# Optimization experiments

Measured on AMD Instinct MI355X. Metric: run time of the kernel, lower is better.

Reference implementation:

```python
import jax, jax.numpy as jnp
import numpy as np

B, N, P2, D, L, K = 256, 256, 64, 128, 2, 9  # batch, nodes, patch^2, embed_dim, vig blocks, knn edges
FFN = 4 * D


def _ln(x, g, b, eps=1e-5):
    m = jnp.mean(x, -1, keepdims=True)
    v = jnp.mean((x - m) ** 2, -1, keepdims=True)
    return (x - m) / jnp.sqrt(v + eps) * g + b


def _lrelu(x):
    return jnp.where(x >= 0, x, 0.01 * x)


def _vig_block(x, mask, mf, fc1_w, fc1_b, conv_w, conv_b, fc2_w, fc2_b, f1_w, f1_b, f2_w, f2_b):
    # Grapher: fc1 -> dynamic kNN -> max-relative graph conv -> fc2, residual
    sc = x
    h = x @ fc1_w + fc1_b  # [B,N,D]
    # pairwise squared distances in feature space; masked nodes excluded as neighbors
    x2 = jnp.sum(h * h, -1)
    d2 = x2[:, :, None] + x2[:, None, :] - 2.0 * jnp.einsum('bnd,bmd->bnm', h, h)
    d2 = jnp.where(mask[:, None, :], d2, 1e10)
    _, idx = jax.lax.top_k(-d2, K)  # [B,N,K] nearest-neighbor indices (non-diff)
    Bq, Nq, Dq = h.shape
    hj = jnp.take_along_axis(h, idx.reshape(Bq, Nq * K, 1), axis=1).reshape(Bq, Nq, K, Dq)
    vj = jnp.take_along_axis(mask, idx.reshape(Bq, Nq * K), axis=1).reshape(Bq, Nq, K)
    rel = jnp.where(vj[..., None], hj - h[:, :, None, :], -1e9)
    mrel = jnp.where(vj.any(2)[..., None], rel.max(2), 0.0)  # max-relative aggregation
    h = _lrelu(jnp.concatenate([h, mrel], -1) @ conv_w + conv_b)
    x = (h @ fc2_w + fc2_b) + sc
    # FFN, residual (drop_path = identity at eval)
    sc = x
    x = _lrelu(x @ f1_w + f1_b) @ f2_w + f2_b + sc
    return x * mf


def setup_inputs() -> dict:
    key = jax.random.key(0)
    ks = jax.random.split(key, 32)
    s = 0.02
    d = {
        'nodes_batch': jax.random.normal(ks[0], (B, N, P2), jnp.float32),
        'node_mask': jax.random.randint(ks[1], (B, N), 0, 2) > 0,
        'emb_w1': jax.random.normal(ks[2], (P2, 2 * D), jnp.float32) * s,
        'emb_b1': jnp.zeros((2 * D,), jnp.float32),
        'emb_ln1_g': jnp.ones((2 * D,), jnp.float32),
        'emb_ln1_b': jnp.zeros((2 * D,), jnp.float32),
        'emb_w2': jax.random.normal(ks[3], (2 * D, D), jnp.float32) * s,
        'emb_b2': jnp.zeros((D,), jnp.float32),
        'emb_ln2_g': jnp.ones((D,), jnp.float32),
        'emb_ln2_b': jnp.zeros((D,), jnp.float32),
        'vig_fc1_w': jax.random.normal(ks[4], (L, D, D), jnp.float32) * s,
        'vig_fc1_b': jnp.zeros((L, D), jnp.float32),
        'vig_conv_w': jax.random.normal(ks[5], (L, 2 * D, D), jnp.float32) * s,
        'vig_conv_b': jnp.zeros((L, D), jnp.float32),
        'vig_fc2_w': jax.random.normal(ks[6], (L, D, D), jnp.float32) * s,
        'vig_fc2_b': jnp.zeros((L, D), jnp.float32),
        'vig_ffn1_w': jax.random.normal(ks[7], (L, D, FFN), jnp.float32) * s,
        'vig_ffn1_b': jnp.zeros((L, FFN), jnp.float32),
        'vig_ffn2_w': jax.random.normal(ks[8], (L, FFN, D), jnp.float32) * s,
        'vig_ffn2_b': jnp.zeros((L, D), jnp.float32),
        'out_w1': jax.random.normal(ks[9], (D, 512), jnp.float32) * s,
        'out_b1': jnp.zeros((512,), jnp.float32),
        'out_w2': jax.random.normal(ks[10], (512, 2048), jnp.float32) * s,
        'out_b2': jnp.zeros((2048,), jnp.float32),
    }
    return d


def reference(nodes_batch, node_mask, emb_w1, emb_b1, emb_ln1_g, emb_ln1_b, emb_w2, emb_b2,
              emb_ln2_g, emb_ln2_b, vig_fc1_w, vig_fc1_b, vig_conv_w, vig_conv_b,
              vig_fc2_w, vig_fc2_b, vig_ffn1_w, vig_ffn1_b, vig_ffn2_w, vig_ffn2_b,
              out_w1, out_b1, out_w2, out_b2):
    mf = node_mask[..., None].astype(nodes_batch.dtype)  # [B,N,1]
    # node embed MLP
    x = _lrelu(_ln(nodes_batch @ emb_w1 + emb_b1, emb_ln1_g, emb_ln1_b))
    x = _ln(x @ emb_w2 + emb_b2, emb_ln2_g, emb_ln2_b)
    x = x * mf
    for l in range(L):
        x = _vig_block(x, node_mask, mf,
                       vig_fc1_w[l], vig_fc1_b[l], vig_conv_w[l], vig_conv_b[l],
                       vig_fc2_w[l], vig_fc2_b[l], vig_ffn1_w[l], vig_ffn1_b[l],
                       vig_ffn2_w[l], vig_ffn2_b[l])
    # masked mean pool
    sum_feat = (x * mf).sum(1)
    num_feat = jnp.maximum(mf.sum(1), 1.0)
    g = sum_feat / num_feat
    return _lrelu(g @ out_w1 + out_b1) @ out_w2 + out_b2
```

## Files before the change

kernel.cpp:

```cpp
#include <hip/hip_runtime.h>
#include <cstdint>

#define BB    256
#define NNODE 256
#define PP2   64
#define DD    128
#define LLAY  2
#define KNN   9
#define FFND  512
#define BNROWS (BB*NNODE)

#define LRELU_(v) ((v) >= 0.f ? (v) : 0.01f*(v))

enum { ACT_NONE = 0, ACT_LRELU = 1 };

typedef short  short8_t  __attribute__((ext_vector_type(8)));
typedef float  f32x4     __attribute__((ext_vector_type(4)));
typedef unsigned short us4 __attribute__((ext_vector_type(4)));
typedef unsigned short us8 __attribute__((ext_vector_type(8)));

__device__ inline unsigned short f2bf(float x) {
    unsigned u = __float_as_uint(x);
    unsigned r = (u + 0x7FFFu + ((u >> 16) & 1u)) >> 16;
    return (unsigned short)r;
}
__device__ inline float bf2f(unsigned short h) {
    return __uint_as_float(((unsigned)h) << 16);
}

__device__ inline void gload16(const void* src, void* dst) {
    __builtin_amdgcn_global_load_lds(
        (const __attribute__((address_space(1))) void*)src,
        (__attribute__((address_space(3))) void*)dst, 16, 0, 0);
}

template<int ROWS, int WAVES>
__device__ inline void stage64g(const unsigned short* __restrict__ g, size_t rowbase,
                                int Kel, int k0, unsigned short* lds, int w, int lane)
{
    constexpr int PER = (ROWS*128/1024) / WAVES;
    #pragma unroll
    for (int i = 0; i < PER; ++i) {
        const int inst = w + i*WAVES;
        const unsigned o  = (unsigned)inst*1024u + (unsigned)lane*16u;
        const int      r  = (int)(o >> 7);
        const unsigned cb = o & 127u;
        const unsigned cs = cb ^ ((unsigned)(r & 7) << 4);
        gload16((const char*)(g + (rowbase + (size_t)r)*(size_t)Kel + k0) + cs,
                (char*)lds + (size_t)inst*1024u);
    }
}

__device__ inline short8_t frag64(const unsigned short* lds, int r, int cb) {
    return *reinterpret_cast<const short8_t*>(
        (const char*)lds + (size_t)r*128 + (unsigned)(cb ^ ((r & 7) << 4)));
}

__device__ inline us8 read8sw(const unsigned short* lds, int r, unsigned cb) {
    return *reinterpret_cast<const us8*>(
        (const char*)lds + (size_t)r*128 + (cb ^ ((unsigned)(r & 7) << 4)));
}

__device__ inline unsigned grp16_min_u32(unsigned v) {
    unsigned t;
    t = (unsigned)__builtin_amdgcn_update_dpp(-1, (int)v, 0xB1,  0xF, 0xF, false); v = t < v ? t : v;
    t = (unsigned)__builtin_amdgcn_update_dpp(-1, (int)v, 0x4E,  0xF, 0xF, false); v = t < v ? t : v;
    t = (unsigned)__builtin_amdgcn_update_dpp(-1, (int)v, 0x124, 0xF, 0xF, false); v = t < v ? t : v;
    t = (unsigned)__builtin_amdgcn_update_dpp(-1, (int)v, 0x128, 0xF, 0xF, false); v = t < v ? t : v;
    return v;
}

__device__ inline float dpp_rowsum16(float v) {
    float t;
    t = __uint_as_float((unsigned)__builtin_amdgcn_update_dpp(0, (int)__float_as_uint(v), 0x111, 0xF, 0xF, false)); v += t;
    t = __uint_as_float((unsigned)__builtin_amdgcn_update_dpp(0, (int)__float_as_uint(v), 0x112, 0xF, 0xF, false)); v += t;
    t = __uint_as_float((unsigned)__builtin_amdgcn_update_dpp(0, (int)__float_as_uint(v), 0x114, 0xF, 0xF, false)); v += t;
    t = __uint_as_float((unsigned)__builtin_amdgcn_update_dpp(0, (int)__float_as_uint(v), 0x118, 0xF, 0xF, false)); v += t;
    return v;
}

#define WAITB0  { asm volatile("s_waitcnt vmcnt(0)" ::: "memory");  __builtin_amdgcn_s_barrier(); asm volatile("" ::: "memory"); }
#define WAITB4  { asm volatile("s_waitcnt vmcnt(4)" ::: "memory");  __builtin_amdgcn_s_barrier(); asm volatile("" ::: "memory"); }
#define WAITB6  { asm volatile("s_waitcnt vmcnt(6)" ::: "memory");  __builtin_amdgcn_s_barrier(); asm volatile("" ::: "memory"); }
#define WAITBL4 { asm volatile("s_waitcnt vmcnt(4) lgkmcnt(0)" ::: "memory"); __builtin_amdgcn_s_barrier(); asm volatile("" ::: "memory"); }

template<int ACT, bool RES, bool MASK, bool OUTF, bool OUTB, bool OUTS>
__global__ __launch_bounds__(256)
void bgemm_k(const unsigned short* __restrict__ A,
             const unsigned short* __restrict__ W,
             const float* __restrict__ bias,
             const float* __restrict__ resp,
             const int* __restrict__ mask,
             float* __restrict__ Cf, unsigned short* __restrict__ Cb,
             unsigned short* Ohi, unsigned short* Olo,
             int M, int N, int K)
{
    __shared__ __align__(16) unsigned short As[128*64];
    __shared__ __align__(16) unsigned short Bs[128*64];

    const int tid  = threadIdx.x;
    const int lane = tid & 63;
    const int w    = tid >> 6;
    const int wr   = w >> 1, wc = w & 1;
    const int row0 = blockIdx.x * 128;
    const int col0 = blockIdx.y * 128;
    const int l15  = lane & 15;
    const int ko   = lane >> 4;

    f32x4 acc[4][4];
    #pragma unroll
    for (int m = 0; m < 4; ++m)
        #pragma unroll
        for (int n = 0; n < 4; ++n) acc[m][n] = (f32x4){0.f,0.f,0.f,0.f};

    for (int k0 = 0; k0 < K; k0 += 64) {
        stage64g<128,4>(A, (size_t)row0, K, k0, As, w, lane);
        stage64g<128,4>(W, (size_t)col0, K, k0, Bs, w, lane);
        __syncthreads();
        #pragma unroll
        for (int ks = 0; ks < 2; ++ks) {
            short8_t aF[4], bF[4];
            #pragma unroll
            for (int m = 0; m < 4; ++m)
                aF[m] = frag64(As, wr*64 + m*16 + l15, ks*64 + ko*16);
            #pragma unroll
            for (int n = 0; n < 4; ++n)
                bF[n] = frag64(Bs, wc*64 + n*16 + l15, ks*64 + ko*16);
            #pragma unroll
            for (int m = 0; m < 4; ++m)
                #pragma unroll
                for (int n = 0; n < 4; ++n)
                    acc[m][n] = __builtin_amdgcn_mfma_f32_16x16x32_bf16(aF[m], bF[n], acc[m][n], 0, 0, 0);
        }
        __syncthreads();
    }

    #pragma unroll
    for (int m = 0; m < 4; ++m) {
        const int rbase = row0 + wr*64 + m*16 + ko*4;
        #pragma unroll
        for (int n = 0; n < 4; ++n) {
            const int col = col0 + wc*64 + n*16 + l15;
            const float bv = bias[col];
            #pragma unroll
            for (int r = 0; r < 4; ++r) {
                const int row = rbase + r;
                float v = acc[m][n][r] + bv;
                if constexpr (ACT == ACT_LRELU) v = LRELU_(v);
                if constexpr (RES)  v += resp[(size_t)row*N + col];
                if constexpr (MASK) v *= (mask[row] != 0) ? 1.f : 0.f;
                if constexpr (OUTF) Cf[(size_t)row*N + col] = v;
                if constexpr (OUTB) Cb[(size_t)row*N + col] = f2bf(v);
                if constexpr (OUTS) {
                    unsigned short h = f2bf(v);
                    Ohi[(size_t)row*N + col] = h;
                    Olo[(size_t)row*N + col] = f2bf(v - bf2f(h));
                }
            }
        }
    }
}

template<int WR, int WC, bool DO_LRELU, bool MASKMUL, int MODE, bool AF32>
__global__ __launch_bounds__(WR*WC*64)
void bgemm_ln_k(const void* __restrict__ Ap,
                const unsigned short* __restrict__ W,
                const float* __restrict__ bias,
                const float* __restrict__ gam,
                const float* __restrict__ bet,
                const int* __restrict__ mask,
                void* __restrict__ outv,
                unsigned short* __restrict__ ohi, unsigned short* __restrict__ olo,
                int K)
{
    constexpr int BM = WR*64;
    constexpr int BN = WC*64;
    constexpr int THREADS = WR*WC*64;
    constexpr int WAVES = THREADS/64;
    __shared__ __align__(16) unsigned short As[BM*64];
    __shared__ __align__(16) unsigned short Bs[BN*64];
    __shared__ float red_s[WC][BM];
    __shared__ float red_q[WC][BM];
    __shared__ float mu_l[BM];
    __shared__ float rs_l[BM];

    const int tid  = threadIdx.x;
    const int lane = tid & 63;
    const int w    = tid >> 6;
    const int wr   = w / WC, wc = w % WC;
    const int row0 = blockIdx.x * BM;
    const int l15  = lane & 15;
    const int ko   = lane >> 4;

    f32x4 acc[4][4];
    #pragma unroll
    for (int m = 0; m < 4; ++m)
        #pragma unroll
        for (int n = 0; n < 4; ++n) acc[m][n] = (f32x4){0.f,0.f,0.f,0.f};

    for (int k0 = 0; k0 < K; k0 += 64) {
        if constexpr (AF32) {
            const float* Af = (const float*)Ap;
            constexpr int CH = (BM*8)/THREADS;
            #pragma unroll
            for (int i = 0; i < CH; ++i) {
                const int q = i*THREADS + tid;
                const unsigned o  = (unsigned)q*16u;
                const int      r  = (int)(o >> 7);
                const unsigned cb = o & 127u;
                const unsigned cs = cb ^ ((unsigned)(r & 7) << 4);
                const float* src = Af + (size_t)(row0 + r)*K + k0 + (cs >> 1);
                const float4 f0 = *reinterpret_cast<const float4*>(src);
                const float4 f1 = *reinterpret_cast<const float4*>(src + 4);
                short8_t v;
                v[0]=(short)f2bf(f0.x); v[1]=(short)f2bf(f0.y); v[2]=(short)f2bf(f0.z); v[3]=(short)f2bf(f0.w);
                v[4]=(short)f2bf(f1.x); v[5]=(short)f2bf(f1.y); v[6]=(short)f2bf(f1.z); v[7]=(short)f2bf(f1.w);
                *reinterpret_cast<short8_t*>((char*)As + o) = v;
            }
        } else {
            stage64g<BM,WAVES>((const unsigned short*)Ap, (size_t)row0, K, k0, As, w, lane);
        }
        stage64g<BN,WAVES>(W, 0, K, k0, Bs, w, lane);
        __syncthreads();
        #pragma unroll
        for (int ks = 0; ks < 2; ++ks) {
            short8_t aF[4], bF[4];
            #pragma unroll
            for (int m = 0; m < 4; ++m)
                aF[m] = frag64(As, wr*64 + m*16 + l15, ks*64 + ko*16);
            #pragma unroll
            for (int n = 0; n < 4; ++n)
                bF[n] = frag64(Bs, wc*64 + n*16 + l15, ks*64 + ko*16);
            #pragma unroll
            for (int m = 0; m < 4; ++m)
                #pragma unroll
                for (int n = 0; n < 4; ++n)
                    acc[m][n] = __builtin_amdgcn_mfma_f32_16x16x32_bf16(aF[m], bF[n], acc[m][n], 0, 0, 0);
        }
        __syncthreads();
    }

    float bv[4];
    #pragma unroll
    for (int n = 0; n < 4; ++n) bv[n] = bias[wc*64 + n*16 + l15];
    #pragma unroll
    for (int m = 0; m < 4; ++m)
        #pragma unroll
        for (int n = 0; n < 4; ++n)
            #pragma unroll
            for (int r = 0; r < 4; ++r) acc[m][n][r] += bv[n];

    #pragma unroll
    for (int m = 0; m < 4; ++m) {
        #pragma unroll
        for (int r = 0; r < 4; ++r) {
            float s = acc[m][0][r] + acc[m][1][r] + acc[m][2][r] + acc[m][3][r];
            float q = acc[m][0][r]*acc[m][0][r] + acc[m][1][r]*acc[m][1][r]
                    + acc[m][2][r]*acc[m][2][r] + acc[m][3][r]*acc[m][3][r];
            s = dpp_rowsum16(s);
            q = dpp_rowsum16(q);
            if (l15 == 15) {
                int rl = wr*64 + m*16 + ko*4 + r;
                red_s[wc][rl] = s;
                red_q[wc][rl] = q;
            }
        }
    }
    __syncthreads();
    if (tid < BM) {
        float s = 0.f, q = 0.f;
        #pragma unroll
        for (int c2 = 0; c2 < WC; ++c2) { s += red_s[c2][tid]; q += red_q[c2][tid]; }
        float mu  = s * (1.0f/BN);
        float var = q * (1.0f/BN) - mu*mu;
        mu_l[tid] = mu;
        rs_l[tid] = rsqrtf(fmaxf(var, 0.f) + 1e-5f);
    }
    __syncthreads();

    float gm[4], bt[4];
    #pragma unroll
    for (int n = 0; n < 4; ++n) {
        int col = wc*64 + n*16 + l15;
        gm[n] = gam[col]; bt[n] = bet[col];
    }
    #pragma unroll
    for (int m = 0; m < 4; ++m) {
        #pragma unroll
        for (int r = 0; r < 4; ++r) {
            const int rl  = wr*64 + m*16 + ko*4 + r;
            const int row = row0 + rl;
            const float mu = mu_l[rl], rs = rs_l[rl];
            float mf = 1.f;
            if constexpr (MASKMUL) mf = (mask[row] != 0) ? 1.f : 0.f;
            #pragma unroll
            for (int n = 0; n < 4; ++n) {
                const int col = wc*64 + n*16 + l15;
                float y = (acc[m][n][r] - mu) * rs * gm[n] + bt[n];
                if constexpr (DO_LRELU) y = LRELU_(y);
                if constexpr (MASKMUL)  y *= mf;
                if constexpr (MODE == 1) {
                    ((unsigned short*)outv)[(size_t)row*BN + col] = f2bf(y);
                } else {
                    unsigned short h = f2bf(y);
                    ohi[(size_t)row*BN + col] = h;
                    olo[(size_t)row*BN + col] = f2bf(y - bf2f(h));
                }
            }
        }
    }
}

__global__ __launch_bounds__(256)
void fc1mm_k(const unsigned short* __restrict__ Ahi, const unsigned short* __restrict__ Alo,
             const unsigned short* __restrict__ Bhi, const unsigned short* __restrict__ Blo,
             const float* __restrict__ bias,
             unsigned short* __restrict__ Ohi, unsigned short* __restrict__ Olo,
             float* __restrict__ x2out)
{
    __shared__ __align__(16) unsigned short As[128*64];
    __shared__ __align__(16) unsigned short Bs[128*64];
    __shared__ float red_q[2][128];

    const int tid  = threadIdx.x;
    const int lane = tid & 63;
    const int w    = tid >> 6;
    const int wr   = w >> 1, wc = w & 1;
    const int row0 = blockIdx.x * 128;
    const int l15  = lane & 15;
    const int ko   = lane >> 4;

    f32x4 acc[4][4];
    #pragma unroll
    for (int m = 0; m < 4; ++m)
        #pragma unroll
        for (int n = 0; n < 4; ++n) acc[m][n] = (f32x4){0.f,0.f,0.f,0.f};

    for (int kk = 0; kk < 384; kk += 64) {
        const int p  = kk >> 7;
        const int kl = kk & 127;
        const unsigned short* Ap2 = (p == 1) ? Alo : Ahi;
        const unsigned short* Bp2 = (p == 2) ? Blo : Bhi;
        stage64g<128,4>(Ap2, (size_t)row0, DD, kl, As, w, lane);
        stage64g<128,4>(Bp2, 0, DD, kl, Bs, w, lane);
        __syncthreads();
        #pragma unroll
        for (int ks = 0; ks < 2; ++ks) {
            short8_t aF[4], bF[4];
            #pragma unroll
            for (int m = 0; m < 4; ++m)
                aF[m] = frag64(As, wr*64 + m*16 + l15, ks*64 + ko*16);
            #pragma unroll
            for (int n = 0; n < 4; ++n)
                bF[n] = frag64(Bs, wc*64 + n*16 + l15, ks*64 + ko*16);
            #pragma unroll
            for (int m = 0; m < 4; ++m)
                #pragma unroll
                for (int n = 0; n < 4; ++n)
                    acc[m][n] = __builtin_amdgcn_mfma_f32_16x16x32_bf16(aF[m], bF[n], acc[m][n], 0, 0, 0);
        }
        __syncthreads();
    }

    float qacc[4][4];
    #pragma unroll
    for (int m = 0; m < 4; ++m) {
        const int rbase = row0 + wr*64 + m*16 + ko*4;
        #pragma unroll
        for (int r = 0; r < 4; ++r) qacc[m][r] = 0.f;
        #pragma unroll
        for (int n = 0; n < 4; ++n) {
            const int col = wc*64 + n*16 + l15;
            const float bv = bias[col];
            #pragma unroll
            for (int r = 0; r < 4; ++r) {
                const int row = rbase + r;
                float v = acc[m][n][r] + bv;
                unsigned short h = f2bf(v);
                unsigned short l = f2bf(v - bf2f(h));
                Ohi[(size_t)row*DD + col] = h;
                Olo[(size_t)row*DD + col] = l;
                float vv = bf2f(h) + bf2f(l);
                qacc[m][r] += vv*vv;
            }
        }
    }
    #pragma unroll
    for (int m = 0; m < 4; ++m)
        #pragma unroll
        for (int r = 0; r < 4; ++r) {
            float q = dpp_rowsum16(qacc[m][r]);
            if (l15 == 15) red_q[wc][wr*64 + m*16 + ko*4 + r] = q;
        }
    __syncthreads();
    if (tid < 128) x2out[row0 + tid] = red_q[0][tid] + red_q[1][tid];
}

__global__ __launch_bounds__(1024)
void dist_topk_gather_k(const unsigned short* __restrict__ hhi,
                        const unsigned short* __restrict__ hlo,
                        const int* __restrict__ mask,
                        const float* __restrict__ x2,
                        unsigned short* __restrict__ cat)
{
    __shared__ __align__(16) unsigned short BsH[2][NNODE*64];
    __shared__ __align__(16) unsigned short BsL[2][NNODE*64];
    __shared__ unsigned char idx_s[NNODE*KNN];
    __shared__ unsigned char msk_s[NNODE];

    const int b    = blockIdx.x;
    const int tid  = threadIdx.x;
    const int lane = tid & 63;
    const int w    = tid >> 6;
    const int l15  = lane & 15;
    const int g    = lane >> 4;

    const unsigned short* Hhi = hhi + (size_t)b*NNODE*DD;
    const unsigned short* Hlo = hlo + (size_t)b*NNODE*DD;
    const float* x2b = x2 + b*NNODE;
    const int*   mkb = mask + b*NNODE;

    stage64g<NNODE,16>(Hhi, 0, DD, 0,  &BsH[0][0], w, lane);
    stage64g<NNODE,16>(Hhi, 0, DD, 64, &BsH[1][0], w, lane);
    stage64g<NNODE,16>(Hlo, 0, DD, 0,  &BsL[0][0], w, lane);
    stage64g<NNODE,16>(Hlo, 0, DD, 64, &BsL[1][0], w, lane);
    if (tid < NNODE) msk_s[tid] = (mkb[tid] != 0) ? 1 : 0;
    __syncthreads();

    const int arow = w*16 + l15;

    f32x4 acc[16];
    #pragma unroll
    for (int n = 0; n < 16; ++n) acc[n] = (f32x4){0.f,0.f,0.f,0.f};

    __builtin_amdgcn_s_setprio(1);
    #pragma unroll
    for (int kt = 0; kt < 2; ++kt) {
        #pragma unroll
        for (int ks = 0; ks < 2; ++ks) {
            short8_t aH = frag64(&BsH[kt][0], arow, ks*64 + g*16);
            short8_t aL = frag64(&BsL[kt][0], arow, ks*64 + g*16);
            #pragma unroll
            for (int n = 0; n < 16; ++n) {
                int brow = n*16 + l15;
                short8_t bH = frag64(&BsH[kt][0], brow, ks*64 + g*16);
                short8_t bL = frag64(&BsL[kt][0], brow, ks*64 + g*16);
                acc[n] = __builtin_amdgcn_mfma_f32_16x16x32_bf16(aH, bH, acc[n], 0, 0, 0);
                acc[n] = __builtin_amdgcn_mfma_f32_16x16x32_bf16(aL, bH, acc[n], 0, 0, 0);
                acc[n] = __builtin_amdgcn_mfma_f32_16x16x32_bf16(aH, bL, acc[n], 0, 0, 0);
            }
        }
    }
    __builtin_amdgcn_s_setprio(0);

    float x2c[16]; unsigned mk[16];
    #pragma unroll
    for (int n = 0; n < 16; ++n) {
        int col = n*16 + l15;
        x2c[n] = x2b[col];
        mk[n]  = (unsigned)msk_s[col];
    }

    #pragma unroll
    for (int r = 0; r < 4; ++r) {
        const int lrow = w*16 + g*4 + r;
        const float x2r = x2b[lrow];
        unsigned key[16];
        #pragma unroll
        for (int n = 0; n < 16; ++n) {
            float v = x2r + x2c[n] - 2.0f*acc[n][r];
            if (!mk[n]) v = 1e10f;
            unsigned u = __float_as_uint(v);
            u = (u & 0x80000000u) ? ~u : (u | 0x80000000u);
            key[n] = (u & 0xFFFFFF00u) | (unsigned)(n*16 + l15);
        }
        for (int it = 0; it < KNN; ++it) {
            unsigned a0 = key[0]  < key[1]  ? key[0]  : key[1];
            unsigned a1 = key[2]  < key[3]  ? key[2]  : key[3];
            unsigned a2 = key[4]  < key[5]  ? key[4]  : key[5];
            unsigned a3 = key[6]  < key[7]  ? key[6]  : key[7];
            unsigned a4 = key[8]  < key[9]  ? key[8]  : key[9];
            unsigned a5 = key[10] < key[11] ? key[10] : key[11];
            unsigned a6 = key[12] < key[13] ? key[12] : key[13];
            unsigned a7 = key[14] < key[15] ? key[14] : key[15];
            unsigned b0 = a0 < a1 ? a0 : a1;
            unsigned b1 = a2 < a3 ? a2 : a3;
            unsigned b2 = a4 < a5 ? a4 : a5;
            unsigned b3 = a6 < a7 ? a6 : a7;
            unsigned c0 = b0 < b1 ? b0 : b1;
            unsigned c1 = b2 < b3 ? b2 : b3;
            unsigned lmin = c0 < c1 ? c0 : c1;
            unsigned gmin = grp16_min_u32(lmin);
            if (l15 == 0) idx_s[lrow*KNN + it] = (unsigned char)(gmin & 0xFFu);
            #pragma unroll
            for (int n = 0; n < 16; ++n)
                if (key[n] == gmin) key[n] = 0xFFFFFFFFu;
        }
    }

    const int gi = lane & 7;
    const unsigned cb = (unsigned)(gi * 16);
    #pragma unroll
    for (int kt = 0; kt < 2; ++kt) {
        #pragma unroll
        for (int p = 0; p < 2; ++p) {
            const int rl = w*16 + p*8 + (lane >> 3);
            us8 h8 = read8sw(&BsH[kt][0], rl, cb);
            us8 l8 = read8sw(&BsL[kt][0], rl, cb);
            float hi[8], m[8];
            #pragma unroll
            for (int d = 0; d < 8; ++d) { hi[d] = bf2f(h8[d]) + bf2f(l8[d]); m[d] = -1e9f; }
            bool any = false;
            #pragma unroll
            for (int q = 0; q < KNN; ++q) {
                int j = idx_s[rl*KNN + q];
                if (msk_s[j]) {
                    any = true;
                    us8 a = read8sw(&BsH[kt][0], j, cb);
                    us8 o = read8sw(&BsL[kt][0], j, cb);
                    #pragma unroll
                    for (int d = 0; d < 8; ++d)
                        m[d] = fmaxf(m[d], bf2f(a[d]) + bf2f(o[d]) - hi[d]);
                }
            }
            us8 o1, o2;
            #pragma unroll
            for (int d = 0; d < 8; ++d) {
                o1[d] = f2bf(hi[d]);
                o2[d] = any ? f2bf(m[d]) : (unsigned short)0;
            }
            const size_t rowbase = (size_t)(b*NNODE + rl)*(2*DD);
            const int c0 = kt*64 + gi*8;
            *reinterpret_cast<us8*>(&cat[rowbase + c0])      = o1;
            *reinterpret_cast<us8*>(&cat[rowbase + DD + c0]) = o2;
        }
    }
}

__global__ __launch_bounds__(256)
void conv_ffn_k(const unsigned short* __restrict__ cat,
                const unsigned short* __restrict__ Wc,
                const float* __restrict__ cb,
                const unsigned short* __restrict__ W2c,
                const float* __restrict__ fb,
                const unsigned short* __restrict__ W1,
                const float* __restrict__ b1,
                const unsigned short* __restrict__ W2f,
                const float* __restrict__ b2,
                const int* __restrict__ mask,
                unsigned short* xhi,
                unsigned short* xlo)
{
    __shared__ __align__(16) unsigned short Bs[3][128*64];
    __shared__ __align__(16) unsigned short h2s[2][64*64];
    __shared__ __align__(16) unsigned short Xs[2][64*64];

    const int tid  = threadIdx.x;
    const int lane = tid & 63;
    const int w    = tid >> 6;
    const int row0 = blockIdx.x * 64;
    const int l15  = lane & 15;
    const int ko   = lane >> 4;

    auto issueB = [&](int t) {
        unsigned short* buf = &Bs[t % 3][0];
        if (t < 4)      stage64g<128,4>(Wc,  0, 256, t*64, buf, w, lane);
        else if (t < 6) stage64g<128,4>(W2c, 0, 128, (t-4)*64, buf, w, lane);
        else {
            int c = (t-6) >> 2, j = (t-6) & 3;
            if (j < 2) stage64g<128,4>(W1, (size_t)(c*128), DD, j*64, buf, w, lane);
            else       stage64g<128,4>(W2f, 0, FFND, c*128 + (j-2)*64, buf, w, lane);
        }
    };

    #define MM8(ATILE, BTILE, ACC)                                              \
        { __builtin_amdgcn_s_setprio(1);                                        \
          _Pragma("unroll")                                                     \
          for (int ks = 0; ks < 2; ++ks) {                                      \
            short8_t aF[4], bF[2];                                              \
            _Pragma("unroll")                                                   \
            for (int m = 0; m < 4; ++m) aF[m] = frag64(ATILE, m*16 + l15, ks*64 + ko*16); \
            _Pragma("unroll")                                                   \
            for (int n = 0; n < 2; ++n) bF[n] = frag64(BTILE, w*32 + n*16 + l15, ks*64 + ko*16); \
            _Pragma("unroll")                                                   \
            for (int m = 0; m < 4; ++m)                                         \
              _Pragma("unroll")                                                 \
              for (int n = 0; n < 2; ++n)                                       \
                ACC[m][n] = __builtin_amdgcn_mfma_f32_16x16x32_bf16(aF[m], bF[n], ACC[m][n], 0, 0, 0); } \
          __builtin_amdgcn_s_setprio(0); }

    #define H2WRITE(ACC, BPTR, DST)                                             \
        { const int kt_ = w >> 1;                                               \
          _Pragma("unroll")                                                     \
          for (int n = 0; n < 2; ++n) {                                         \
            const int col_ = w*32 + n*16 + l15;                                 \
            const float bv_ = (BPTR)[col_];                                     \
            const unsigned bc_ = (unsigned)(((w & 1)*32 + n*16 + l15) * 2);     \
            _Pragma("unroll")                                                   \
            for (int m = 0; m < 4; ++m)                                         \
              _Pragma("unroll")                                                 \
              for (int r = 0; r < 4; ++r) {                                     \
                const int row_ = m*16 + ko*4 + r;                               \
                float v_ = LRELU_(ACC[m][n][r] + bv_);                          \
                *(unsigned short*)((char*)&(DST)[kt_][0] + row_*128             \
                    + (bc_ ^ ((unsigned)(row_ & 7) << 4))) = f2bf(v_); } } }

    stage64g<64,4>(cat, (size_t)row0, 256, 0,  &Xs[0][0], w, lane);
    issueB(0);
    stage64g<64,4>(cat, (size_t)row0, 256, 64, &Xs[1][0], w, lane);
    issueB(1);

    f32x4 accc[4][2];
    #pragma unroll
    for (int m = 0; m < 4; ++m)
        #pragma unroll
        for (int n = 0; n < 2; ++n) accc[m][n] = (f32x4){0.f,0.f,0.f,0.f};

    WAITB6;
    issueB(2);
    MM8(&Xs[0][0], &Bs[0][0], accc);

    WAITB4;
    stage64g<64,4>(cat, (size_t)row0, 256, 128, &Xs[0][0], w, lane);
    issueB(3);
    MM8(&Xs[1][0], &Bs[1][0], accc);

    WAITB4;
    stage64g<64,4>(cat, (size_t)row0, 256, 192, &Xs[1][0], w, lane);
    issueB(4);
    MM8(&Xs[0][0], &Bs[2][0], accc);

    WAITB4;
    issueB(5);
    MM8(&Xs[1][0], &Bs[0][0], accc);
    H2WRITE(accc, cb, h2s);

    f32x4 accx[4][2];
    #pragma unroll
    for (int m = 0; m < 4; ++m)
        #pragma unroll
        for (int n = 0; n < 2; ++n) accx[m][n] = (f32x4){0.f,0.f,0.f,0.f};

    WAITBL4;
    issueB(6);
    MM8(&h2s[0][0], &Bs[1][0], accx);

    WAITB4;
    issueB(7);
    MM8(&h2s[1][0], &Bs[2][0], accx);
    float xn[4][2][4];
    {
        const int kt = w >> 1;
        #pragma unroll
        for (int n = 0; n < 2; ++n) {
            const int col = w*32 + n*16 + l15;
            const float bv = fb[col];
            const unsigned bc = (unsigned)(((w & 1)*32 + n*16 + l15) * 2);
            #pragma unroll
            for (int m = 0; m < 4; ++m) {
                #pragma unroll
                for (int r = 0; r < 4; ++r) {
                    const int row = m*16 + ko*4 + r;
                    const size_t gix = (size_t)(row0 + row)*DD + col;
                    float res = bf2f(xhi[gix]) + bf2f(xlo[gix]);
                    float v = accx[m][n][r] + bv + res;
                    xn[m][n][r] = v;
                    *(unsigned short*)((char*)&Xs[kt][0] + row*128
                        + (bc ^ ((unsigned)(row & 7) << 4))) = f2bf(v);
                }
            }
        }
    }

    f32x4 acc2[4][2];
    #pragma unroll
    for (int m = 0; m < 4; ++m)
        #pragma unroll
        for (int n = 0; n < 2; ++n) acc2[m][n] = (f32x4){0.f,0.f,0.f,0.f};

    #pragma unroll
    for (int c = 0; c < 4; ++c) {
        const int tb = 6 + c*4;
        f32x4 acc1[4][2];
        #pragma unroll
        for (int m = 0; m < 4; ++m)
            #pragma unroll
            for (int n = 0; n < 2; ++n) acc1[m][n] = (f32x4){0.f,0.f,0.f,0.f};

        if (c == 0) { WAITBL4; } else { WAITB4; }
        if (tb+2 <= 21) issueB(tb+2);
        MM8(&Xs[0][0], &Bs[tb % 3][0], acc1);

        WAITB4;
        if (tb+3 <= 21) issueB(tb+3);
        MM8(&Xs[1][0], &Bs[(tb+1) % 3][0], acc1);
        H2WRITE(acc1, b1 + c*128, h2s);

        WAITBL4;
        if (tb+4 <= 21) issueB(tb+4);
        MM8(&h2s[0][0], &Bs[(tb+2) % 3][0], acc2);

        if (c == 3) { WAITB0; } else { WAITB4; }
        if (tb+5 <= 21) issueB(tb+5);
        MM8(&h2s[1][0], &Bs[(tb+3) % 3][0], acc2);
    }

    #pragma unroll
    for (int m = 0; m < 4; ++m) {
        const int rbase = row0 + m*16 + ko*4;
        #pragma unroll
        for (int n = 0; n < 2; ++n) {
            const int col = w*32 + n*16 + l15;
            const float bv = b2[col];
            #pragma unroll
            for (int r = 0; r < 4; ++r) {
                const int row = rbase + r;
                float v = acc2[m][n][r] + bv + xn[m][n][r];
                v *= (mask[row] != 0) ? 1.f : 0.f;
                unsigned short h = f2bf(v);
                xhi[(size_t)row*DD + col] = h;
                xlo[(size_t)row*DD + col] = f2bf(v - bf2f(h));
            }
        }
    }
    #undef MM8
    #undef H2WRITE
}

__global__ __launch_bounds__(128)
void pool_k(const unsigned short* __restrict__ xhi, const unsigned short* __restrict__ xlo,
            const int* __restrict__ mask,
            float* __restrict__ g, unsigned short* __restrict__ gbf)
{
    const int b = blockIdx.x, c = threadIdx.x;
    float s = 0.f; int cnt = 0;
    for (int n = 0; n < NNODE; ++n) {
        const size_t ix = ((size_t)b*NNODE + n)*DD + c;
        s += bf2f(xhi[ix]) + bf2f(xlo[ix]);
        cnt += (mask[b*NNODE + n] != 0) ? 1 : 0;
    }
    float v = s / fmaxf((float)cnt, 1.0f);
    g[b*DD + c] = v;
    gbf[b*DD + c] = f2bf(v);
}

__global__ __launch_bounds__(256)
void prep_all_k(const float* __restrict__ emb_w1, const float* __restrict__ emb_w2,
                const float* __restrict__ conv_w, const float* __restrict__ fc2_w,
                const float* __restrict__ f1_w,   const float* __restrict__ f2_w,
                const float* __restrict__ fc1_w,  const float* __restrict__ ow1,
                const float* __restrict__ ow2,
                unsigned short* __restrict__ emb_w1t, unsigned short* __restrict__ emb_w2t,
                unsigned short* __restrict__ conv_wt, unsigned short* __restrict__ fc2_wt,
                unsigned short* __restrict__ ffn1_wt, unsigned short* __restrict__ ffn2_wt,
                unsigned short* __restrict__ fc1_wthi, unsigned short* __restrict__ fc1_wtlo,
                unsigned short* __restrict__ ow1t, unsigned short* __restrict__ ow2t)
{
    __shared__ float tile[32][33];
    const int tx = threadIdx.x & 31, ty = threadIdx.x >> 5;

    int bid = blockIdx.x;
    const float* src = nullptr; unsigned short* dst = nullptr; unsigned short* dlo = nullptr;
    int K = 0, N = 0;
    do {
        if (bid < 16)  { src = emb_w1; dst = emb_w1t; K = 64;  N = 256; break; }  bid -= 16;
        if (bid < 32)  { src = emb_w2; dst = emb_w2t; K = 256; N = 128; break; }  bid -= 32;
        if (bid < 64)  { int l = bid >> 5; bid &= 31;
                         src = conv_w + (size_t)l*256*128; dst = conv_wt + (size_t)l*128*256;
                         K = 256; N = 128; break; }                               bid -= 64;
        if (bid < 32)  { int l = bid >> 4; bid &= 15;
                         src = fc2_w + (size_t)l*128*128; dst = fc2_wt + (size_t)l*128*128;
                         K = 128; N = 128; break; }                               bid -= 32;
        if (bid < 128) { int l = bid >> 6; bid &= 63;
                         src = f1_w + (size_t)l*128*512; dst = ffn1_wt + (size_t)l*512*128;
                         K = 128; N = 512; break; }                               bid -= 128;
        if (bid < 128) { int l = bid >> 6; bid &= 63;
                         src = f2_w + (size_t)l*512*128; dst = ffn2_wt + (size_t)l*128*512;
                         K = 512; N = 128; break; }                               bid -= 128;
        if (bid < 32)  { int l = bid >> 4; bid &= 15;
                         src = fc1_w + (size_t)l*128*128;
                         dst = fc1_wthi + (size_t)l*128*128; dlo = fc1_wtlo + (size_t)l*128*128;
                         K = 128; N = 128; break; }                               bid -= 32;
        if (bid < 64)  { src = ow1; dst = ow1t; K = 128; N = 512; break; }        bid -= 64;
        { src = ow2; dst = ow2t; K = 512; N = 2048; }
    } while (0);

    const int nbx = N / 32;
    const int bx = bid % nbx, by = bid / nbx;
    const int k0 = by*32, n0 = bx*32;

    #pragma unroll
    for (int i = ty; i < 32; i += 8)
        tile[i][tx] = src[(size_t)(k0+i)*N + n0+tx];
    __syncthreads();
    #pragma unroll
    for (int i = ty; i < 32; i += 8) {
        float v = tile[tx][i];
        unsigned short h = f2bf(v);
        dst[(size_t)(n0+i)*K + k0+tx] = h;
        if (dlo) dlo[(size_t)(n0+i)*K + k0+tx] = f2bf(v - bf2f(h));
    }
}

extern "C" void kernel_launch(void* const* d_in, const int* in_sizes, int n_in,
                              void* d_out, int out_size, void* d_ws, size_t ws_size,
                              hipStream_t stream)
{
    const float* nodes  = (const float*)d_in[0];
    const int*   maskp  = (const int*)  d_in[1];
    const float* emb_w1 = (const float*)d_in[2];
    const float* emb_b1 = (const float*)d_in[3];
    const float* ln1_g  = (const float*)d_in[4];
    const float* ln1_b  = (const float*)d_in[5];
    const float* emb_w2 = (const float*)d_in[6];
    const float* emb_b2 = (const float*)d_in[7];
    const float* ln2_g  = (const float*)d_in[8];
    const float* ln2_b  = (const float*)d_in[9];
    const float* fc1_w  = (const float*)d_in[10];
    const float* fc1_b  = (const float*)d_in[11];
    const float* conv_w = (const float*)d_in[12];
    const float* conv_b = (const float*)d_in[13];
    const float* fc2_w  = (const float*)d_in[14];
    const float* fc2_b  = (const float*)d_in[15];
    const float* f1_w   = (const float*)d_in[16];
    const float* f1_b   = (const float*)d_in[17];
    const float* f2_w   = (const float*)d_in[18];
    const float* f2_b   = (const float*)d_in[19];
    const float* ow1    = (const float*)d_in[20];
    const float* ob1    = (const float*)d_in[21];
    const float* ow2    = (const float*)d_in[22];
    const float* ob2    = (const float*)d_in[23];
    float* out = (float*)d_out;

    char* base = (char*)d_ws;
    char*  H   = base + (size_t)BNROWS*DD*4;
    char*  BIG = H + (size_t)BNROWS*DD*4;
    float*          x2    = (float*)(BIG + (size_t)BNROWS*2*DD*4);
    float*          g     = (float*)(x2 + BNROWS);
    unsigned short* g_bf  = (unsigned short*)(g + BB*DD);
    unsigned short* hid2_bf = g_bf + BB*DD;
    unsigned short* wbuf  = hid2_bf + BB*FFND;

    unsigned short* x_hi   = (unsigned short*)H;
    unsigned short* x_lo   = x_hi + (size_t)BNROWS*DD;
    unsigned short* t256_bf= (unsigned short*)base;
    unsigned short* cat_bf = (unsigned short*)BIG;
    unsigned short* h_hi   = (unsigned short*)(BIG + (size_t)BNROWS*DD*2);
    unsigned short* h_lo   = h_hi + (size_t)BNROWS*DD;

    unsigned short* emb_w1t  = wbuf;
    unsigned short* emb_w2t  = emb_w1t + 256*64;
    unsigned short* conv_wt  = emb_w2t + 128*256;
    unsigned short* fc2_wt   = conv_wt + 2*128*256;
    unsigned short* ffn1_wt  = fc2_wt  + 2*128*128;
    unsigned short* ffn2_wt  = ffn1_wt + 2*512*128;
    unsigned short* fc1_wthi = ffn2_wt + 2*128*512;
    unsigned short* fc1_wtlo = fc1_wthi + 2*128*128;
    unsigned short* ow1t     = fc1_wtlo + 2*128*128;
    unsigned short* ow2t     = ow1t + 512*128;

    const dim3 blk(256);

    prep_all_k<<<1520, blk, 0, stream>>>(
        emb_w1, emb_w2, conv_w, fc2_w, f1_w, f2_w, fc1_w, ow1, ow2,
        emb_w1t, emb_w2t, conv_wt, fc2_wt, ffn1_wt, ffn2_wt,
        fc1_wthi, fc1_wtlo, ow1t, ow2t);

    bgemm_ln_k<2,4,true,false,1,true>
        <<<dim3(BNROWS/128), dim3(512), 0, stream>>>
        (nodes, emb_w1t, emb_b1, ln1_g, ln1_b, nullptr, t256_bf, nullptr, nullptr, PP2);
    bgemm_ln_k<2,2,false,true,2,false>
        <<<dim3(BNROWS/128), dim3(256), 0, stream>>>
        (t256_bf, emb_w2t, emb_b2, ln2_g, ln2_b, maskp, nullptr, x_hi, x_lo, 2*DD);

    for (int l = 0; l < LLAY; ++l) {
        const float* fc1b = fc1_b + (size_t)l*DD;
        const float* cb   = conv_b + (size_t)l*DD;
        const float* fc2b = fc2_b + (size_t)l*DD;
        const float* b1   = f1_b + (size_t)l*FFND;
        const float* b2   = f2_b + (size_t)l*DD;

        fc1mm_k<<<dim3(BNROWS/128), blk, 0, stream>>>
            (x_hi, x_lo, fc1_wthi + (size_t)l*DD*DD, fc1_wtlo + (size_t)l*DD*DD,
             fc1b, h_hi, h_lo, x2);
        dist_topk_gather_k<<<dim3(BB), dim3(1024), 0, stream>>>
            (h_hi, h_lo, maskp, x2, cat_bf);
        conv_ffn_k<<<dim3(BNROWS/64), blk, 0, stream>>>
            (cat_bf, conv_wt + (size_t)l*DD*2*DD, cb,
             fc2_wt + (size_t)l*DD*DD, fc2b,
             ffn1_wt + (size_t)l*FFND*DD, b1,
             ffn2_wt + (size_t)l*DD*FFND, b2, maskp,
             x_hi, x_lo);
    }

    pool_k<<<BB, 128, 0, stream>>>(x_hi, x_lo, maskp, g, g_bf);
    bgemm_k<ACT_LRELU,false,false,false,true,false>
        <<<dim3(BB/128, 512/128), blk, 0, stream>>>
        (g_bf, ow1t, ob1, nullptr, nullptr, nullptr, hid2_bf, nullptr, nullptr, BB, 512, DD);
    bgemm_k<ACT_NONE,false,false,true,false,false>
        <<<dim3(BB/128, 2048/128), blk, 0, stream>>>
        (hid2_bf, ow2t, ob2, nullptr, nullptr, out, nullptr, nullptr, nullptr, BB, 2048, 512);
}
```

Before: 292.3 us.

## Fuse fc1 GEMM into per-graph distance/top-k/gather kernel

The separate fc1 GEMM kernel is removed. Each per-batch 1024-thread block now loads x (hi/lo bf16) into LDS, computes h = x@fc1_w+b with MFMA against staged weight tiles, and writes the result back into the same swizzled LDS buffers. Squared norms stay in shared memory, so the global round trip for h_hi, h_lo and x2 and one launch per layer go away. In exchange it adds LDS pressure from an extra weight tile and runs fc1 with only 256 blocks, each doing serial weight staging with barriers.

```diff
diff --git a/kernel.cpp b/kernel.cpp
--- a/kernel.cpp
+++ b/kernel.cpp
@@ -311,100 +311,19 @@
     }
 }
 
-__global__ __launch_bounds__(256)
-void fc1mm_k(const unsigned short* __restrict__ Ahi, const unsigned short* __restrict__ Alo,
-             const unsigned short* __restrict__ Bhi, const unsigned short* __restrict__ Blo,
-             const float* __restrict__ bias,
-             unsigned short* __restrict__ Ohi, unsigned short* __restrict__ Olo,
-             float* __restrict__ x2out)
-{
-    __shared__ __align__(16) unsigned short As[128*64];
-    __shared__ __align__(16) unsigned short Bs[128*64];
-    __shared__ float red_q[2][128];
-
-    const int tid  = threadIdx.x;
-    const int lane = tid & 63;
-    const int w    = tid >> 6;
-    const int wr   = w >> 1, wc = w & 1;
-    const int row0 = blockIdx.x * 128;
-    const int l15  = lane & 15;
-    const int ko   = lane >> 4;
-
-    f32x4 acc[4][4];
-    #pragma unroll
-    for (int m = 0; m < 4; ++m)
-        #pragma unroll
-        for (int n = 0; n < 4; ++n) acc[m][n] = (f32x4){0.f,0.f,0.f,0.f};
-
-    for (int kk = 0; kk < 384; kk += 64) {
-        const int p  = kk >> 7;
-        const int kl = kk & 127;
-        const unsigned short* Ap2 = (p == 1) ? Alo : Ahi;
-        const unsigned short* Bp2 = (p == 2) ? Blo : Bhi;
-        stage64g<128,4>(Ap2, (size_t)row0, DD, kl, As, w, lane);
-        stage64g<128,4>(Bp2, 0, DD, kl, Bs, w, lane);
-        __syncthreads();
-        #pragma unroll
-        for (int ks = 0; ks < 2; ++ks) {
-            short8_t aF[4], bF[4];
-            #pragma unroll
-            for (int m = 0; m < 4; ++m)
-                aF[m] = frag64(As, wr*64 + m*16 + l15, ks*64 + ko*16);
-            #pragma unroll
-            for (int n = 0; n < 4; ++n)
-                bF[n] = frag64(Bs, wc*64 + n*16 + l15, ks*64 + ko*16);
-            #pragma unroll
-            for (int m = 0; m < 4; ++m)
-                #pragma unroll
-                for (int n = 0; n < 4; ++n)
-                    acc[m][n] = __builtin_amdgcn_mfma_f32_16x16x32_bf16(aF[m], bF[n], acc[m][n], 0, 0, 0);
-        }
-        __syncthreads();
-    }
-
-    float qacc[4][4];
-    #pragma unroll
-    for (int m = 0; m < 4; ++m) {
-        const int rbase = row0 + wr*64 + m*16 + ko*4;
-        #pragma unroll
-        for (int r = 0; r < 4; ++r) qacc[m][r] = 0.f;
-        #pragma unroll
-        for (int n = 0; n < 4; ++n) {
-            const int col = wc*64 + n*16 + l15;
-            const float bv = bias[col];
-            #pragma unroll
-            for (int r = 0; r < 4; ++r) {
-                const int row = rbase + r;
-                float v = acc[m][n][r] + bv;
-                unsigned short h = f2bf(v);
-                unsigned short l = f2bf(v - bf2f(h));
-                Ohi[(size_t)row*DD + col] = h;
-                Olo[(size_t)row*DD + col] = l;
-                float vv = bf2f(h) + bf2f(l);
-                qacc[m][r] += vv*vv;
-            }
-        }
-    }
-    #pragma unroll
-    for (int m = 0; m < 4; ++m)
-        #pragma unroll
-        for (int r = 0; r < 4; ++r) {
-            float q = dpp_rowsum16(qacc[m][r]);
-            if (l15 == 15) red_q[wc][wr*64 + m*16 + ko*4 + r] = q;
-        }
-    __syncthreads();
-    if (tid < 128) x2out[row0 + tid] = red_q[0][tid] + red_q[1][tid];
-}
-
 __global__ __launch_bounds__(1024)
-void dist_topk_gather_k(const unsigned short* __restrict__ hhi,
-                        const unsigned short* __restrict__ hlo,
-                        const int* __restrict__ mask,
-                        const float* __restrict__ x2,
-                        unsigned short* __restrict__ cat)
+void fc1_dist_topk_gather_k(const unsigned short* __restrict__ xhi,
+                            const unsigned short* __restrict__ xlo,
+                            const unsigned short* __restrict__ Whi,
+                            const unsigned short* __restrict__ Wlo,
+                            const float* __restrict__ fc1b,
+                            const int* __restrict__ mask,
+                            unsigned short* __restrict__ cat)
 {
     __shared__ __align__(16) unsigned short BsH[2][NNODE*64];
     __shared__ __align__(16) unsigned short BsL[2][NNODE*64];
+    __shared__ __align__(16) unsigned short Ws[128*64];
+    __shared__ float x2s[NNODE];
     __shared__ unsigned char idx_s[NNODE*KNN];
     __shared__ unsigned char msk_s[NNODE];
 
@@ -415,19 +334,73 @@
     const int l15  = lane & 15;
     const int g    = lane >> 4;
 
-    const unsigned short* Hhi = hhi + (size_t)b*NNODE*DD;
-    const unsigned short* Hlo = hlo + (size_t)b*NNODE*DD;
-    const float* x2b = x2 + b*NNODE;
-    const int*   mkb = mask + b*NNODE;
-
-    stage64g<NNODE,16>(Hhi, 0, DD, 0,  &BsH[0][0], w, lane);
-    stage64g<NNODE,16>(Hhi, 0, DD, 64, &BsH[1][0], w, lane);
-    stage64g<NNODE,16>(Hlo, 0, DD, 0,  &BsL[0][0], w, lane);
-    stage64g<NNODE,16>(Hlo, 0, DD, 64, &BsL[1][0], w, lane);
+    const unsigned short* Xhi = xhi + (size_t)b*NNODE*DD;
+    const unsigned short* Xlo = xlo + (size_t)b*NNODE*DD;
+    const int* mkb = mask + b*NNODE;
+
+    stage64g<NNODE,16>(Xhi, 0, DD, 0,  &BsH[0][0], w, lane);
+    stage64g<NNODE,16>(Xhi, 0, DD, 64, &BsH[1][0], w, lane);
+    stage64g<NNODE,16>(Xlo, 0, DD, 0,  &BsL[0][0], w, lane);
+    stage64g<NNODE,16>(Xlo, 0, DD, 64, &BsL[1][0], w, lane);
     if (tid < NNODE) msk_s[tid] = (mkb[tid] != 0) ? 1 : 0;
     __syncthreads();
 
     const int arow = w*16 + l15;
+
+    f32x4 hacc[8];
+    #pragma unroll
+    for (int n = 0; n < 8; ++n) hacc[n] = (f32x4){0.f,0.f,0.f,0.f};
+
+    #pragma unroll
+    for (int wp = 0; wp < 4; ++wp) {
+        const unsigned short* Wsrc = (wp < 2) ? Whi : Wlo;
+        const int kt = wp & 1;
+        stage64g<128,16>(Wsrc, 0, DD, kt*64, Ws, w, lane);
+        __syncthreads();
+        const int nAv = (wp < 2) ? 2 : 1;
+        for (int av = 0; av < nAv; ++av) {
+            const unsigned short* At = (av == 0) ? &BsH[kt][0] : &BsL[kt][0];
+            #pragma unroll
+            for (int ks = 0; ks < 2; ++ks) {
+                short8_t aF = frag64(At, arow, ks*64 + g*16);
+                #pragma unroll
+                for (int n = 0; n < 8; ++n) {
+                    short8_t bF = frag64(Ws, n*16 + l15, ks*64 + g*16);
+                    hacc[n] = __builtin_amdgcn_mfma_f32_16x16x32_bf16(aF, bF, hacc[n], 0, 0, 0);
+                }
+            }
+        }
+        __syncthreads();
+    }
+
+    {
+        float qr[4] = {0.f, 0.f, 0.f, 0.f};
+        #pragma unroll
+        for (int n = 0; n < 8; ++n) {
+            const int col = n*16 + l15;
+            const float bv = fc1b[col];
+            const int kt = col >> 6;
+            const unsigned bc = (unsigned)((col & 63) * 2);
+            #pragma unroll
+            for (int r = 0; r < 4; ++r) {
+                const int row = w*16 + g*4 + r;
+                float v = hacc[n][r] + bv;
+                unsigned short hh = f2bf(v);
+                unsigned short hl = f2bf(v - bf2f(hh));
+                const unsigned off = (unsigned)(row*128) + (bc ^ ((unsigned)(row & 7) << 4));
+                *(unsigned short*)((char*)&BsH[kt][0] + off) = hh;
+                *(unsigned short*)((char*)&BsL[kt][0] + off) = hl;
+                float vv = bf2f(hh) + bf2f(hl);
+                qr[r] += vv*vv;
+            }
+        }
+        #pragma unroll
+        for (int r = 0; r < 4; ++r) {
+            float q = dpp_rowsum16(qr[r]);
+            if (l15 == 15) x2s[w*16 + g*4 + r] = q;
+        }
+    }
+    __syncthreads();
 
     f32x4 acc[16];
     #pragma unroll
@@ -457,14 +430,14 @@
     #pragma unroll
     for (int n = 0; n < 16; ++n) {
         int col = n*16 + l15;
-        x2c[n] = x2b[col];
+        x2c[n] = x2s[col];
         mk[n]  = (unsigned)msk_s[col];
     }
 
     #pragma unroll
     for (int r = 0; r < 4; ++r) {
         const int lrow = w*16 + g*4 + r;
-        const float x2r = x2b[lrow];
+        const float x2r = x2s[lrow];
         unsigned key[16];
         #pragma unroll
         for (int n = 0; n < 16; ++n) {
@@ -835,8 +808,7 @@
     char* base = (char*)d_ws;
     char*  H   = base + (size_t)BNROWS*DD*4;
     char*  BIG = H + (size_t)BNROWS*DD*4;
-    float*          x2    = (float*)(BIG + (size_t)BNROWS*2*DD*4);
-    float*          g     = (float*)(x2 + BNROWS);
+    float*          g     = (float*)(BIG + (size_t)BNROWS*2*DD*4);
     unsigned short* g_bf  = (unsigned short*)(g + BB*DD);
     unsigned short* hid2_bf = g_bf + BB*DD;
     unsigned short* wbuf  = hid2_bf + BB*FFND;
@@ -845,8 +817,6 @@
     unsigned short* x_lo   = x_hi + (size_t)BNROWS*DD;
     unsigned short* t256_bf= (unsigned short*)base;
     unsigned short* cat_bf = (unsigned short*)BIG;
-    unsigned short* h_hi   = (unsigned short*)(BIG + (size_t)BNROWS*DD*2);
-    unsigned short* h_lo   = h_hi + (size_t)BNROWS*DD;
 
     unsigned short* emb_w1t  = wbuf;
     unsigned short* emb_w2t  = emb_w1t + 256*64;
@@ -880,11 +850,9 @@
         const float* b1   = f1_b + (size_t)l*FFND;
         const float* b2   = f2_b + (size_t)l*DD;
 
-        fc1mm_k<<<dim3(BNROWS/128), blk, 0, stream>>>
+        fc1_dist_topk_gather_k<<<dim3(BB), dim3(1024), 0, stream>>>
             (x_hi, x_lo, fc1_wthi + (size_t)l*DD*DD, fc1_wtlo + (size_t)l*DD*DD,
-             fc1b, h_hi, h_lo, x2);
-        dist_topk_gather_k<<<dim3(BB), dim3(1024), 0, stream>>>
-            (h_hi, h_lo, maskp, x2, cat_bf);
+             fc1b, maskp, cat_bf);
         conv_ffn_k<<<dim3(BNROWS/64), blk, 0, stream>>>
             (cat_bf, conv_wt + (size_t)l*DD*2*DD, cb,
              fc2_wt + (size_t)l*DD*DD, fc2b,
```

After: 273.1 us. 1.07x faster.
